# Optimization experiments

Hardware: AMD Instinct MI355X
Metric: run time of the kernel (lower is better)

The kernel has to match this reference:

```python
import jax, jax.numpy as jnp
import numpy as np
import math

V, D, H, NH, LE, LD = 32000, 256, 1024, 8, 2, 2
B, T = 4, 512


def qlinear(x, W, b):
    # x: [..., Din, 4]; W: [4, Dout, Din] (r,i,j,k); b: [Dout, 4] or None
    r, i, j, k = x[..., 0], x[..., 1], x[..., 2], x[..., 3]
    Wr, Wi, Wj, Wk = W[0], W[1], W[2], W[3]
    f = lambda a, M: jnp.einsum('...d,od->...o', a, M)
    ro = f(r, Wr) - f(i, Wi) - f(j, Wj) - f(k, Wk)
    io = f(r, Wi) + f(i, Wr) + f(j, Wk) - f(k, Wj)
    jo = f(r, Wj) - f(i, Wk) + f(j, Wr) + f(k, Wi)
    ko = f(r, Wk) + f(i, Wj) - f(j, Wi) + f(k, Wr)
    out = jnp.stack([ro, io, jo, ko], axis=-1)
    return out + b if b is not None else out


def modrelu(x, bias):
    # x: [..., F, 4]; bias: [F]
    norm = jnp.linalg.norm(x, axis=-1)
    scale = jax.nn.relu(norm + bias) / (norm + 1e-6)
    return x * scale[..., None]


def qnorm(x, g, beta):
    # normalize each quaternion (last dim of size 4) to unit norm
    n = jnp.sqrt(jnp.sum(x * x, axis=-1, keepdims=True) + 1e-6)
    return g * (x / n) + beta


def qattn(q, k, v, W, b, mask, nh):
    # W: [4(proj q,k,v,out), 4(comp), D, D]; b: [4, D, 4]
    def split(x):
        Bq, Tq, Dq, _ = x.shape
        return x.reshape(Bq, Tq, nh, Dq // nh, 4).transpose(0, 2, 1, 3, 4)
    qh = split(qlinear(q, W[0], b[0]))
    kh = split(qlinear(k, W[1], b[1]))
    vh = split(qlinear(v, W[2], b[2]))
    hd = qh.shape[3]
    s = jnp.einsum('bhqfd,bhkfd->bhqk', qh, kh) / math.sqrt(hd * 4)
    if mask is not None:
        s = jnp.where(mask[:, None] == 0, -jnp.inf, s)
    w = jax.nn.softmax(s, axis=-1)
    o = jnp.einsum('bhqk,bhkfd->bhqfd', w, vh)
    Bq, h, Tq, f, _ = o.shape
    o = o.transpose(0, 2, 1, 3, 4).reshape(Bq, Tq, h * f, 4)
    return qlinear(o, W[3], b[3])


def qff(x, W1, b1, mbias, W2, b2):
    return qlinear(modrelu(qlinear(x, W1, b1), mbias), W2, b2)


def qembed(ids, emb):
    d = emb.shape[-1]
    scale = 1.0 / 10000.0 ** (jnp.arange(d, dtype=jnp.float32) / d)
    r = emb[0][ids]
    i = emb[1][ids] * scale
    j = emb[2][ids] * scale
    k = emb[3][ids] * scale
    n = jnp.sqrt(r * r + i * i + j * j + k * k + 1e-6)
    return jnp.stack([r / n, i / n, j / n, k / n], axis=-1)


def rope(x):
    t, d = x.shape[1], x.shape[2]
    inv = 1.0 / 10000.0 ** (jnp.arange(0, d, 2, dtype=jnp.float32) / d)
    fr = jnp.arange(t, dtype=jnp.float32)[:, None] * inv[None, :]
    ang = jnp.concatenate([jnp.sin(fr), jnp.cos(fr)], axis=-1)  # [T, D]
    return x * ang[None, :, :, None]


def setup_inputs():
    key = jax.random.key(0)
    ks = jax.random.split(key, 12)
    n = lambda k, s: jax.random.normal(k, s, jnp.float32) * 0.02
    src = jax.random.randint(ks[0], (B, T), 0, V)
    tgt = jax.random.randint(ks[1], (B, T), 0, V)
    tgt_mask = jnp.broadcast_to(jnp.tril(jnp.ones((T, T), jnp.int32)), (B, T, T))
    return dict(
        src=src, tgt=tgt, tgt_mask=tgt_mask,
        emb=n(ks[2], (4, V, D)),
        enc_attn_W=n(ks[3], (LE, 4, 4, D, D)), enc_attn_b=jnp.zeros((LE, 4, D, 4)),
        enc_norm_g=jnp.ones((LE, 2, D, 4)), enc_norm_b=jnp.zeros((LE, 2, D, 4)),
        enc_ff_W1=n(ks[4], (LE, 4, H, D)), enc_ff_b1=jnp.zeros((LE, H, 4)),
        enc_ff_mod=jnp.zeros((LE, H)),
        enc_ff_W2=n(ks[5], (LE, 4, D, H)), enc_ff_b2=jnp.zeros((LE, D, 4)),
        dec_sa_W=n(ks[6], (LD, 4, 4, D, D)), dec_sa_b=jnp.zeros((LD, 4, D, 4)),
        dec_ca_W=n(ks[7], (LD, 4, 4, D, D)), dec_ca_b=jnp.zeros((LD, 4, D, 4)),
        dec_norm_g=jnp.ones((LD, 3, D, 4)), dec_norm_b=jnp.zeros((LD, 3, D, 4)),
        dec_ff_W1=n(ks[8], (LD, 4, H, D)), dec_ff_b1=jnp.zeros((LD, H, 4)),
        dec_ff_mod=jnp.zeros((LD, H)),
        dec_ff_W2=n(ks[9], (LD, 4, D, H)), dec_ff_b2=jnp.zeros((LD, D, 4)),
        fc_W=n(ks[10], (V, D)), fc_b=jnp.zeros((V,)),
    )


def reference(src, tgt, tgt_mask, emb,
              enc_attn_W, enc_attn_b, enc_norm_g, enc_norm_b,
              enc_ff_W1, enc_ff_b1, enc_ff_mod, enc_ff_W2, enc_ff_b2,
              dec_sa_W, dec_sa_b, dec_ca_W, dec_ca_b, dec_norm_g, dec_norm_b,
              dec_ff_W1, dec_ff_b1, dec_ff_mod, dec_ff_W2, dec_ff_b2,
              fc_W, fc_b):
    x_src = rope(qembed(src, emb))
    x_tgt = rope(qembed(tgt, emb))
    # encoder stack
    m = x_src
    for l in range(LE):
        m = qnorm(m + qattn(m, m, m, enc_attn_W[l], enc_attn_b[l], None, NH), enc_norm_g[l, 0], enc_norm_b[l, 0])
        m = qnorm(m + qff(m, enc_ff_W1[l], enc_ff_b1[l], enc_ff_mod[l], enc_ff_W2[l], enc_ff_b2[l]), enc_norm_g[l, 1], enc_norm_b[l, 1])
    # decoder stack
    x = x_tgt
    for l in range(LD):
        x = qnorm(x + qattn(x, x, x, dec_sa_W[l], dec_sa_b[l], tgt_mask, NH), dec_norm_g[l, 0], dec_norm_b[l, 0])
        x = qnorm(x + qattn(x, m, m, dec_ca_W[l], dec_ca_b[l], None, NH), dec_norm_g[l, 1], dec_norm_b[l, 1])
        x = qnorm(x + qff(x, dec_ff_W1[l], dec_ff_b1[l], dec_ff_mod[l], dec_ff_W2[l], dec_ff_b2[l]), dec_norm_g[l, 2], dec_norm_b[l, 2])
    real = jnp.linalg.norm(x, axis=-1)  # QuaternionToReal('norm') -> [B, T, D]
    logits = jnp.einsum('btd,vd->btv', real, fc_W) + fc_b
    return logits
```

## Files before the change

kernel.cpp:

```cpp
#include <hip/hip_runtime.h>
#include <math.h>

#define B 4
#define T 512
#define D 256
#define H 1024
#define NH 8
#define V 32000
#define BT (B*T)
#define LE 2
#define LD 2
#define DIM 1024

typedef __attribute__((ext_vector_type(8))) short s16x8;
typedef __attribute__((ext_vector_type(4))) float f32x4;
typedef __attribute__((address_space(3))) void lds_void;
typedef const __attribute__((address_space(1))) void g_void;

__device__ __forceinline__ ushort f2bf(float x) {
  uint u = __float_as_uint(x);
  return (ushort)((u + 0x7fffu + ((u >> 16) & 1u)) >> 16);
}
__device__ __forceinline__ float bf2f(ushort u) {
  return __uint_as_float(((uint)u) << 16);
}

#define QSCALE 0.08838834764831845f

#define A_CNT  1572864
#define F_CNT  2097152
#define FC_CNT 2048000
#define EMB_CNT (2 * BT * 256)
#define MEGA_TOT (A_CNT + F_CNT + FC_CNT + EMB_CNT)
#define WSTEP  1048576
#define FFW    4194304

__device__ __forceinline__ void qexpand_write(
    const float* __restrict__ src, ushort* __restrict__ dst,
    int o, int d, int Din, int P) {
  float w0 = src[(size_t)o * Din + d];
  float w1 = src[P + (size_t)o * Din + d];
  float w2 = src[2 * (size_t)P + (size_t)o * Din + d];
  float w3 = src[3 * (size_t)P + (size_t)o * Din + d];
  int K4 = Din * 4;
  size_t rbase = (size_t)(o * 4) * K4 + d * 4;
  *(ushort4*)(dst + rbase)          = make_ushort4(f2bf(w0), f2bf(-w1), f2bf(-w2), f2bf(-w3));
  *(ushort4*)(dst + rbase + K4)     = make_ushort4(f2bf(w1), f2bf(w0),  f2bf(w3),  f2bf(-w2));
  *(ushort4*)(dst + rbase + 2 * K4) = make_ushort4(f2bf(w2), f2bf(-w3), f2bf(w0),  f2bf(w1));
  *(ushort4*)(dst + rbase + 3 * K4) = make_ushort4(f2bf(w3), f2bf(w2),  f2bf(-w1), f2bf(w0));
}

__global__ __launch_bounds__(256) void mega_expand_kernel(
    const float* __restrict__ encA, const float* __restrict__ decSA,
    const float* __restrict__ decCA,
    const float* __restrict__ eW1, const float* __restrict__ eW2,
    const float* __restrict__ dW1, const float* __restrict__ dW2,
    const float* __restrict__ fcW,
    ushort* __restrict__ WA, ushort* __restrict__ WF, ushort* __restrict__ Wfc,
    const int* __restrict__ srcIds, const int* __restrict__ tgtIds,
    const float* __restrict__ emb,
    float* __restrict__ xsrc, ushort* __restrict__ xbfs,
    float* __restrict__ xtgt, ushort* __restrict__ xbft) {
  int gid = blockIdx.x * 256 + threadIdx.x;
  if (gid < A_CNT) {
    int u = gid >> 18;
    int p = (gid >> 16) & 3;
    int rem = gid & 65535;
    int o = rem >> 8, d = rem & 255;
    const float* base = (u < 2) ? encA + (size_t)u * 1048576
                      : (u < 4) ? decSA + (size_t)(u - 2) * 1048576
                                : decCA + (size_t)(u - 4) * 1048576;
    qexpand_write(base + (size_t)p * 262144,
                  WA + ((size_t)u * 4 + p) * WSTEP, o, d, 256, 65536);
  } else if (gid < A_CNT + F_CNT) {
    int idx = gid - A_CNT;
    int layer = idx >> 19;
    int w12 = (idx >> 18) & 1;
    int rem = idx & 262143;
    const float* w1b = (layer < 2) ? eW1 + (size_t)layer * 1048576
                                   : dW1 + (size_t)(layer - 2) * 1048576;
    const float* w2b = (layer < 2) ? eW2 + (size_t)layer * 1048576
                                   : dW2 + (size_t)(layer - 2) * 1048576;
    ushort* dst = WF + (size_t)layer * 2 * FFW + (size_t)w12 * FFW;
    if (w12 == 0) {
      int o = rem >> 8, d = rem & 255;
      qexpand_write(w1b, dst, o, d, 256, 262144);
    } else {
      int o = rem >> 10, d = rem & 1023;
      qexpand_write(w2b, dst, o, d, 1024, 262144);
    }
  } else if (gid < A_CNT + F_CNT + FC_CNT) {
    int idx = gid - A_CNT - F_CNT;
    float4 v = ((const float4*)fcW)[idx];
    ((ushort4*)Wfc)[idx] = make_ushort4(f2bf(v.x), f2bf(v.y), f2bf(v.z), f2bf(v.w));
  } else if (gid < MEGA_TOT) {
    int idx = gid - A_CNT - F_CNT - FC_CNT;
    int g = idx >> 8, d = idx & 255;
    int isTgt = g >= BT;
    int bt = isTgt ? g - BT : g;
    int id = isTgt ? tgtIds[bt] : srcIds[bt];
    float* out = isTgt ? xtgt : xsrc;
    ushort* outbf = isTgt ? xbft : xbfs;
    int t = bt % T;
    size_t VD = (size_t)V * D;
    float scale = powf(10000.f, -(float)d / (float)D);
    float r = emb[(size_t)id * D + d];
    float i = emb[VD + (size_t)id * D + d] * scale;
    float j = emb[2 * VD + (size_t)id * D + d] * scale;
    float k = emb[3 * VD + (size_t)id * D + d] * scale;
    float n = sqrtf(r * r + i * i + j * j + k * k + 1e-6f);
    float ang;
    if (d < D / 2) {
      float inv = powf(10000.f, -(float)(2 * d) / (float)D);
      ang = sinf((float)t * inv);
    } else {
      float inv = powf(10000.f, -(float)(2 * (d - D / 2)) / (float)D);
      ang = cosf((float)t * inv);
    }
    float s = ang / n;
    size_t base = (size_t)bt * DIM + d * 4;
    float4 q = make_float4(r * s, i * s, j * s, k * s);
    *(float4*)(out + base) = q;
    *(ushort4*)(outbf + base) = make_ushort4(f2bf(q.x), f2bf(q.y), f2bf(q.z), f2bf(q.w));
  }
}

struct GP {
  const ushort* A; const ushort* Aalt; int altStart;
  const ushort* Bt; const float* bias; void* Cv;
  ushort* qo; ushort* ko; ushort* vo;
  float* xres; ushort* xbf; const float* gg; const float* bb;
  const float* modb; ushort* realout;
};

template <int OMODE, int TM, int NBUF>
__global__ __launch_bounds__(256, 4) void gemm_bf16_kernel(
    GP u0, GP u1, int nunits, int nsplit, int N, int K) {
  __shared__ ushort As[NBUF][TM * 32];
  __shared__ ushort Bs[NBUF][128 * 32];
  const int tid = threadIdx.x;
  const int w = tid >> 6, l = tid & 63;
  const int nwg = gridDim.x;
  const int qq = nwg >> 3, rr = nwg & 7;
  const int xcd = blockIdx.x & 7, pos = blockIdx.x >> 3;
  const int wg = (xcd < rr ? xcd * (qq + 1) : rr * (qq + 1) + (xcd - rr) * qq) + pos;
  const int uwg = nwg / (nunits * nsplit);
  const int idx = wg / uwg;
  const int unit = idx / nsplit;
  const int split = idx % nsplit;
  const int wgl = wg % uwg;
  GP U = unit ? u1 : u0;
  const int Ksub = K / nsplit;
  const int kbase = split * Ksub;
  const int nbx = N >> 7;
  const int nby = uwg / nbx;
  const int m0 = (wgl % nby) * TM, n0 = (wgl / nby) * 128;
  const ushort* Ap = (U.altStart && n0 >= U.altStart) ? U.Aalt : U.A;
  const ushort* Btp = U.Bt;
  const int lr = l & 15, lg = l >> 4;
  constexpr int NR = (TM == 128) ? 4 : 2;
  const int wm = (TM == 128) ? (w >> 1) : 0;
  const int wn = (TM == 128) ? (w & 1) : w;
  const int wcol = wn * (NR * 16);
  f32x4 acc[4][NR] = {};
  const int NT = Ksub >> 5;

  auto stage = [&](int t, int buf) {
    int k0 = kbase + (t << 5);
#pragma unroll
    for (int s = 0; s < TM / 64; ++s) {
      int fb = (w * (TM / 64) + s) * 1024;
      int f = fb + l * 16;
      int row = f >> 6, cb = (f & 63) >> 1;
      __builtin_amdgcn_global_load_lds(
          (g_void*)(Ap + (size_t)(m0 + row) * K + k0 + cb),
          (lds_void*)((char*)&As[buf][0] + fb), 16, 0, 0);
    }
#pragma unroll
    for (int s = 0; s < 2; ++s) {
      int fb = (w * 2 + s) * 1024;
      int f = fb + l * 16;
      int row = f >> 6, cb = (f & 63) >> 1;
      __builtin_amdgcn_global_load_lds(
          (g_void*)(Btp + (size_t)(n0 + row) * K + k0 + cb),
          (lds_void*)((char*)&Bs[buf][0] + fb), 16, 0, 0);
    }
  };
  auto compute = [&](int buf) {
    s16x8 af[4], bfr[NR];
#pragma unroll
    for (int mi = 0; mi < 4; ++mi)
      af[mi] = *(const s16x8*)(&As[buf][0] + (wm * 64 + mi * 16 + lr) * 32 + lg * 8);
#pragma unroll
    for (int ni = 0; ni < NR; ++ni)
      bfr[ni] = *(const s16x8*)(&Bs[buf][0] + (wcol + ni * 16 + lr) * 32 + lg * 8);
    __builtin_amdgcn_s_setprio(1);
#pragma unroll
    for (int mi = 0; mi < 4; ++mi)
#pragma unroll
      for (int ni = 0; ni < NR; ++ni)
        acc[mi][ni] = __builtin_amdgcn_mfma_f32_16x16x32_bf16(af[mi], bfr[ni], acc[mi][ni], 0, 0, 0);
    __builtin_amdgcn_s_setprio(0);
  };

  if constexpr (NBUF == 4) {
    stage(0, 0);
    stage(1, 1);
    __syncthreads();
    for (int t = 0; t < NT; t += 2) {
      if (t + 2 < NT) {
        stage(t + 2, (t + 2) & 3);
        stage(t + 3, (t + 3) & 3);
      }
      compute(t & 3);
      compute((t + 1) & 3);
      __syncthreads();
    }
  } else {
    stage(0, 0);
    __syncthreads();
    int cur = 0;
    for (int t = 0; t < NT; ++t) {
      if (t + 1 < NT) stage(t + 1, cur ^ 1);
      compute(cur);
      __syncthreads();
      cur ^= 1;
    }
  }

#pragma unroll
  for (int mi = 0; mi < 4; ++mi) {
#pragma unroll
    for (int ni = 0; ni < NR; ++ni) {
      int row = m0 + wm * 64 + mi * 16 + lg * 4;
      int col = n0 + wcol + ni * 16 + lr;
      f32x4 v = acc[mi][ni];
      if constexpr (OMODE == 0) {
        float bv = U.bias ? U.bias[col] : 0.f;
        float* C = (float*)U.Cv;
#pragma unroll
        for (int r = 0; r < 4; ++r)
          C[(size_t)(row + r) * N + col] = v[r] + bv;
      } else if constexpr (OMODE == 3) {
        float bv = U.bias[col];
        if (col < 2048) {
          ushort* dst = (col < DIM) ? U.qo : U.ko;
          float sc = (col < DIM) ? QSCALE : 1.f;
          int c = col & (DIM - 1);
#pragma unroll
          for (int r = 0; r < 4; ++r)
            dst[(size_t)(row + r) * DIM + c] = f2bf((v[r] + bv) * sc);
        } else {
          int c = col - 2048;
          ushort4 o4 = make_ushort4(f2bf(v[0] + bv), f2bf(v[1] + bv),
                                    f2bf(v[2] + bv), f2bf(v[3] + bv));
          *(ushort4*)&U.vo[((size_t)((row >> 9) << 10) + c) * T + (row & 511)] = o4;
        }
      } else if constexpr (OMODE == 4) {
        float bv = U.bias[col];
        float gv = U.gg[col], bev = U.bb[col];
#pragma unroll
        for (int r = 0; r < 4; ++r) {
          float val = v[r] + bv + U.xres[(size_t)(row + r) * DIM + col];
          float sq = val * val;
          sq += __shfl_xor(sq, 1);
          sq += __shfl_xor(sq, 2);
          float invn = rsqrtf(sq + 1e-6f);
          float res = gv * (val * invn) + bev;
          U.xres[(size_t)(row + r) * DIM + col] = res;
          U.xbf[(size_t)(row + r) * DIM + col] = f2bf(res);
          if (U.realout) {
            float rsq = res * res;
            rsq += __shfl_xor(rsq, 1);
            rsq += __shfl_xor(rsq, 2);
            if ((col & 3) == 0)
              U.realout[(size_t)(row + r) * D + (col >> 2)] = f2bf(sqrtf(rsq));
          }
        }
      } else if constexpr (OMODE == 5) {
        float bv = U.bias[col];
        float mb = U.modb[col >> 2];
        ushort* C = (ushort*)U.Cv;
#pragma unroll
        for (int r = 0; r < 4; ++r) {
          float val = v[r] + bv;
          float sq = val * val;
          sq += __shfl_xor(sq, 1);
          sq += __shfl_xor(sq, 2);
          float norm = sqrtf(sq);
          float scale = fmaxf(norm + mb, 0.f) / (norm + 1e-6f);
          C[(size_t)(row + r) * N + col] = f2bf(val * scale);
        }
      } else {
        ushort* P = (ushort*)U.Cv + (size_t)split * BT * N;
#pragma unroll
        for (int r = 0; r < 4; ++r)
          P[(size_t)(row + r) * N + col] = f2bf(v[r]);
      }
    }
  }
}

__global__ __launch_bounds__(256) void ff2_merge_kernel(
    const ushort* __restrict__ P, const float* __restrict__ bias,
    float* __restrict__ xres, ushort* __restrict__ xbf,
    const float* __restrict__ gg, const float* __restrict__ bb,
    ushort* __restrict__ realo) {
  int idx = blockIdx.x * 256 + threadIdx.x;
  int row = idx >> 8;
  int c4 = (idx & 255) << 2;
  size_t base = (size_t)row * DIM + c4;
  float a0 = 0.f, a1 = 0.f, a2 = 0.f, a3 = 0.f;
#pragma unroll
  for (int sp = 0; sp < 4; ++sp) {
    ushort4 p = *(const ushort4*)(P + (size_t)sp * BT * DIM + base);
    a0 += bf2f(p.x); a1 += bf2f(p.y); a2 += bf2f(p.z); a3 += bf2f(p.w);
  }
  float4 xv = *(float4*)(xres + base);
  float v0 = a0 + bias[c4 + 0] + xv.x;
  float v1 = a1 + bias[c4 + 1] + xv.y;
  float v2 = a2 + bias[c4 + 2] + xv.z;
  float v3 = a3 + bias[c4 + 3] + xv.w;
  float invn = rsqrtf(v0 * v0 + v1 * v1 + v2 * v2 + v3 * v3 + 1e-6f);
  float r0 = gg[c4 + 0] * (v0 * invn) + bb[c4 + 0];
  float r1 = gg[c4 + 1] * (v1 * invn) + bb[c4 + 1];
  float r2 = gg[c4 + 2] * (v2 * invn) + bb[c4 + 2];
  float r3 = gg[c4 + 3] * (v3 * invn) + bb[c4 + 3];
  *(float4*)(xres + base) = make_float4(r0, r1, r2, r3);
  *(ushort4*)(xbf + base) = make_ushort4(f2bf(r0), f2bf(r1), f2bf(r2), f2bf(r3));
  if (realo)
    realo[(size_t)row * D + (c4 >> 2)] =
        f2bf(sqrtf(r0 * r0 + r1 * r1 + r2 * r2 + r3 * r3));
}

__global__ __launch_bounds__(256) void fused_attn_kernel(
    const ushort* __restrict__ qb, const ushort* __restrict__ kb,
    const ushort* __restrict__ vT, ushort* __restrict__ outA,
    int c0, int c1) {
  __shared__ ushort Ks[2][64 * 128];
  __shared__ ushort Vs[2][128 * 64];
  __shared__ ushort Pst[4][1024];
  const int tid = threadIdx.x;
  const int wq = tid >> 6, l = tid & 63;
  const int lr = l & 15, lg = l >> 4;
  const int h = blockIdx.y;
  const int u = blockIdx.z >> 2, b = blockIdx.z & 3;
  const size_t uoff = (size_t)u * ((size_t)BT * DIM);
  const int causal = u ? c1 : c0;
  const int q0 = blockIdx.x * 64 + wq * 16;
  const size_t bT = (size_t)b * T;
  const int hc = h * 128;
  const size_t vrow0 = (size_t)(b * NH + h) * 128;
  const ushort* qbu = qb + uoff;
  const ushort* kbu = kb + uoff;
  const ushort* vTu = vT + uoff;
  ushort* outu = outA + uoff;
  s16x8 qf[4];
#pragma unroll
  for (int ks = 0; ks < 4; ++ks)
    qf[ks] = *(const s16x8*)(qbu + (bT + q0 + lr) * DIM + hc + ks * 32 + lg * 8);
  f32x4 O[8] = {};
  float m[4] = {-3e38f, -3e38f, -3e38f, -3e38f};
  float lac[4] = {0.f, 0.f, 0.f, 0.f};
  const int kend = causal ? (blockIdx.x + 1) * 64 : T;
  const int ntile = kend >> 6;

  auto stageKV = [&](int tile, int buf) {
    int kv0 = tile << 6;
#pragma unroll
    for (int s = 0; s < 4; ++s) {
      int f = s * 4096 + tid * 16;
      int row = f >> 8, g = (f >> 4) & 15;
      int gs = g ^ (row & 7);
      __builtin_amdgcn_global_load_lds(
          (g_void*)(kbu + (bT + kv0 + row) * DIM + hc + gs * 8),
          (lds_void*)((char*)&Ks[buf][0] + f), 16, 0, 0);
    }
#pragma unroll
    for (int s = 0; s < 4; ++s) {
      int f = s * 4096 + tid * 16;
      int row = f >> 7, g = (f >> 4) & 7;
      int gs = g ^ (row & 7);
      __builtin_amdgcn_global_load_lds(
          (g_void*)(vTu + (vrow0 + row) * T + kv0 + gs * 8),
          (lds_void*)((char*)&Vs[buf][0] + f), 16, 0, 0);
    }
  };

  stageKV(0, 0);
  __syncthreads();
  int cur = 0;
  for (int tile = 0; tile < ntile; ++tile) {
    const int kv0 = tile << 6;
    if (tile + 1 < ntile) stageKV(tile + 1, cur ^ 1);
    f32x4 s[4] = {};
#pragma unroll
    for (int ks = 0; ks < 4; ++ks) {
      s16x8 kf[4];
#pragma unroll
      for (int ni = 0; ni < 4; ++ni) {
        int row = ni * 16 + lr;
        int g = (ks * 4 + lg) ^ (row & 7);
        kf[ni] = *(const s16x8*)(&Ks[cur][0] + row * 128 + g * 8);
      }
#pragma unroll
      for (int ni = 0; ni < 4; ++ni)
        s[ni] = __builtin_amdgcn_mfma_f32_16x16x32_bf16(qf[ks], kf[ni], s[ni], 0, 0, 0);
    }
    const bool domask = causal && (kv0 + 63 > q0);
#pragma unroll
    for (int r = 0; r < 4; ++r) {
      const int qrow = q0 + lg * 4 + r;
      float mx = -3e38f;
#pragma unroll
      for (int ni = 0; ni < 4; ++ni) {
        float v = s[ni][r];
        if (domask && (kv0 + ni * 16 + lr > qrow)) v = -3e38f;
        s[ni][r] = v;
        mx = fmaxf(mx, v);
      }
#pragma unroll
      for (int dd = 1; dd < 16; dd <<= 1) mx = fmaxf(mx, __shfl_xor(mx, dd));
      if (__ballot(mx > m[r] + 8.f)) {
        float mn = fmaxf(m[r], mx);
        float alpha = __expf(m[r] - mn);
        m[r] = mn;
        lac[r] *= alpha;
#pragma unroll
        for (int dni = 0; dni < 8; ++dni) O[dni][r] *= alpha;
      }
      float ps = 0.f;
#pragma unroll
      for (int ni = 0; ni < 4; ++ni) {
        float p = __expf(s[ni][r] - m[r]);
        s[ni][r] = p;
        ps += p;
      }
#pragma unroll
      for (int dd = 1; dd < 16; dd <<= 1) ps += __shfl_xor(ps, dd);
      lac[r] += ps;
      const int qloc = lg * 4 + r;
      const int sw = (qloc & 7) << 3;
#pragma unroll
      for (int ni = 0; ni < 4; ++ni)
        Pst[wq][qloc * 64 + ((ni * 16 + lr) ^ sw)] = f2bf(s[ni][r]);
    }
    asm volatile("s_waitcnt lgkmcnt(0)" ::: "memory");
    __builtin_amdgcn_sched_barrier(0);
#pragma unroll
    for (int ks2 = 0; ks2 < 2; ++ks2) {
      s16x8 pa = *(const s16x8*)&Pst[wq][lr * 64 + ((ks2 * 32 + lg * 8) ^ ((lr & 7) << 3))];
#pragma unroll
      for (int dni = 0; dni < 8; ++dni) {
        int row = dni * 16 + lr;
        int g = (ks2 * 4 + lg) ^ (row & 7);
        s16x8 vf = *(const s16x8*)(&Vs[cur][0] + row * 64 + g * 8);
        O[dni] = __builtin_amdgcn_mfma_f32_16x16x32_bf16(pa, vf, O[dni], 0, 0, 0);
      }
    }
    __syncthreads();
    cur ^= 1;
  }
#pragma unroll
  for (int r = 0; r < 4; ++r) {
    float inv = 1.f / lac[r];
    const size_t row = bT + q0 + lg * 4 + r;
#pragma unroll
    for (int dni = 0; dni < 8; ++dni)
      outu[row * DIM + hc + dni * 16 + lr] = f2bf(O[dni][r] * inv);
  }
}

extern "C" void kernel_launch(void* const* d_in, const int* in_sizes, int n_in,
                              void* d_out, int out_size, void* d_ws, size_t ws_size,
                              hipStream_t stream) {
  const int*   src        = (const int*)d_in[0];
  const int*   tgt        = (const int*)d_in[1];
  const float* emb        = (const float*)d_in[3];
  const float* enc_attn_W = (const float*)d_in[4];
  const float* enc_attn_b = (const float*)d_in[5];
  const float* enc_norm_g = (const float*)d_in[6];
  const float* enc_norm_b = (const float*)d_in[7];
  const float* enc_ff_W1  = (const float*)d_in[8];
  const float* enc_ff_b1  = (const float*)d_in[9];
  const float* enc_ff_mod = (const float*)d_in[10];
  const float* enc_ff_W2  = (const float*)d_in[11];
  const float* enc_ff_b2  = (const float*)d_in[12];
  const float* dec_sa_W   = (const float*)d_in[13];
  const float* dec_sa_b   = (const float*)d_in[14];
  const float* dec_ca_W   = (const float*)d_in[15];
  const float* dec_ca_b   = (const float*)d_in[16];
  const float* dec_norm_g = (const float*)d_in[17];
  const float* dec_norm_b = (const float*)d_in[18];
  const float* dec_ff_W1  = (const float*)d_in[19];
  const float* dec_ff_b1  = (const float*)d_in[20];
  const float* dec_ff_mod = (const float*)d_in[21];
  const float* dec_ff_W2  = (const float*)d_in[22];
  const float* dec_ff_b2  = (const float*)d_in[23];
  const float* fc_W       = (const float*)d_in[24];
  const float* fc_b       = (const float*)d_in[25];
  float* out = (float*)d_out;

  const size_t USZ = (size_t)BT * DIM;
  float* ws    = (float*)d_ws;
  float* xsrc  = ws;
  float* xtgt  = xsrc + USZ;
  ushort* xbf_src = (ushort*)(xtgt + USZ);
  ushort* xbf_tgt = xbf_src + USZ;
  ushort* aobf    = xbf_tgt + USZ;
  ushort* qb      = aobf + 2 * USZ;
  ushort* kb      = qb + 2 * USZ;
  ushort* vTb     = kb + 2 * USZ;
  ushort* hbf     = vTb + 2 * USZ;
  ushort* realbf  = hbf + (size_t)BT * H * 4;
  ushort* WA      = realbf + (size_t)BT * D;
  ushort* WF      = WA + (size_t)6 * 4 * WSTEP;
  ushort* Wfc     = WF + (size_t)4 * 2 * FFW;
  ushort* Pff     = Wfc + (size_t)V * D;

  mega_expand_kernel<<<(MEGA_TOT + 255) / 256, 256, 0, stream>>>(
      enc_attn_W, dec_sa_W, dec_ca_W,
      enc_ff_W1, enc_ff_W2, dec_ff_W1, dec_ff_W2, fc_W, WA, WF, Wfc,
      src, tgt, emb, xsrc, xbf_src, xtgt, xbf_tgt);

  GP Z{};

  auto mkQKV = [&](const ushort* Abf, const ushort* Wu, const float* bb, int u) {
    GP g = Z;
    g.A = Abf; g.Bt = Wu; g.bias = bb;
    g.qo = qb + u * USZ; g.ko = kb + u * USZ; g.vo = vTb + u * USZ;
    return g;
  };
  auto mkOP = [&](int u, const ushort* Wu3, const float* bb, float* xres,
                  ushort* xbf, const float* gg, const float* nb, ushort* realo) {
    GP g = Z;
    g.A = aobf + u * USZ; g.Bt = Wu3; g.bias = bb;
    g.xres = xres; g.xbf = xbf; g.gg = gg; g.bb = nb; g.realout = realo;
    return g;
  };

  auto qkv1 = [&](GP g) {
    gemm_bf16_kernel<3, 128, 2><<<384, 256, 0, stream>>>(g, g, 1, 1, 3 * DIM, DIM);
  };
  auto qkv2 = [&](GP g0, GP g1) {
    gemm_bf16_kernel<3, 128, 2><<<768, 256, 0, stream>>>(g0, g1, 2, 1, 3 * DIM, DIM);
  };
  auto op1 = [&](GP g) {
    gemm_bf16_kernel<4, 64, 4><<<256, 256, 0, stream>>>(g, g, 1, 1, DIM, DIM);
  };
  auto op2 = [&](GP g0, GP g1) {
    gemm_bf16_kernel<4, 64, 4><<<512, 256, 0, stream>>>(g0, g1, 2, 1, DIM, DIM);
  };
  auto attn1 = [&](int causal) {
    fused_attn_kernel<<<dim3(T / 64, NH, B), 256, 0, stream>>>(
        qb, kb, vTb, aobf, causal, causal);
  };
  auto ffpair = [&](const ushort* xbf, int layer, const float* b1,
                    const float* mod, const float* b2, float* xres,
                    ushort* xbfo, const float* gg, const float* nb,
                    ushort* realo) {
    const ushort* Wf = WF + (size_t)layer * 2 * FFW;
    GP g1 = Z;
    g1.A = xbf; g1.Bt = Wf; g1.bias = b1; g1.Cv = hbf; g1.modb = mod;
    gemm_bf16_kernel<5, 128, 2><<<512, 256, 0, stream>>>(g1, g1, 1, 1, 4 * H, DIM);
    GP g2 = Z;
    g2.A = hbf; g2.Bt = Wf + FFW; g2.Cv = Pff;
    gemm_bf16_kernel<6, 64, 2><<<1024, 256, 0, stream>>>(g2, g2, 1, 4, DIM, 4 * H);
    ff2_merge_kernel<<<BT, 256, 0, stream>>>(Pff, b2, xres, xbfo, gg, nb, realo);
  };

  {
    GP e = mkQKV(xbf_src, WA + (size_t)(0 * 4) * WSTEP, enc_attn_b, 0);
    GP d = mkQKV(xbf_tgt, WA + (size_t)(2 * 4) * WSTEP, dec_sa_b, 1);
    qkv2(e, d);
    fused_attn_kernel<<<dim3(T / 64, NH, 2 * B), 256, 0, stream>>>(
        qb, kb, vTb, aobf, 0, 1);
    GP eo = mkOP(0, WA + (size_t)(0 * 4 + 3) * WSTEP, enc_attn_b + 3 * DIM,
                 xsrc, xbf_src, enc_norm_g, enc_norm_b, nullptr);
    GP dd = mkOP(1, WA + (size_t)(2 * 4 + 3) * WSTEP, dec_sa_b + 3 * DIM,
                 xtgt, xbf_tgt, dec_norm_g, dec_norm_b, nullptr);
    op2(eo, dd);
  }
  ffpair(xbf_src, 0, enc_ff_b1, enc_ff_mod, enc_ff_b2, xsrc, xbf_src,
         enc_norm_g + 1 * DIM, enc_norm_b + 1 * DIM, nullptr);
  {
    GP e = mkQKV(xbf_src, WA + (size_t)(1 * 4) * WSTEP,
                 enc_attn_b + (size_t)1 * 4 * DIM, 0);
    qkv1(e);
    attn1(0);
    GP eo = mkOP(0, WA + (size_t)(1 * 4 + 3) * WSTEP,
                 enc_attn_b + (size_t)1 * 4 * DIM + 3 * DIM,
                 xsrc, xbf_src, enc_norm_g + 2 * DIM, enc_norm_b + 2 * DIM, nullptr);
    op1(eo);
  }
  ffpair(xbf_src, 1, enc_ff_b1 + (size_t)1 * H * 4, enc_ff_mod + H,
         enc_ff_b2 + DIM, xsrc, xbf_src,
         enc_norm_g + 3 * DIM, enc_norm_b + 3 * DIM, nullptr);

  for (int l = 0; l < LD; ++l) {
    if (l > 0) {
      GP d = mkQKV(xbf_tgt, WA + (size_t)((2 + l) * 4) * WSTEP,
                   dec_sa_b + (size_t)l * 4 * DIM, 0);
      qkv1(d);
      attn1(1);
      GP od = mkOP(0, WA + (size_t)((2 + l) * 4 + 3) * WSTEP,
                   dec_sa_b + (size_t)l * 4 * DIM + 3 * DIM,
                   xtgt, xbf_tgt, dec_norm_g + (size_t)(l * 3) * DIM,
                   dec_norm_b + (size_t)(l * 3) * DIM, nullptr);
      op1(od);
    }
    {
      GP g = mkQKV(xbf_tgt, WA + (size_t)((4 + l) * 4) * WSTEP,
                   dec_ca_b + (size_t)l * 4 * DIM, 0);
      g.Aalt = xbf_src; g.altStart = DIM;
      qkv1(g);
      attn1(0);
      GP og = mkOP(0, WA + (size_t)((4 + l) * 4 + 3) * WSTEP,
                   dec_ca_b + (size_t)l * 4 * DIM + 3 * DIM,
                   xtgt, xbf_tgt, dec_norm_g + (size_t)(l * 3 + 1) * DIM,
                   dec_norm_b + (size_t)(l * 3 + 1) * DIM, nullptr);
      op1(og);
    }
    ffpair(xbf_tgt, 2 + l, dec_ff_b1 + (size_t)l * H * 4,
           dec_ff_mod + (size_t)l * H, dec_ff_b2 + (size_t)l * DIM,
           xtgt, xbf_tgt, dec_norm_g + (size_t)(l * 3 + 2) * DIM,
           dec_norm_b + (size_t)(l * 3 + 2) * DIM,
           (l == LD - 1) ? realbf : nullptr);
  }

  {
    GP g = Z;
    g.A = realbf; g.Bt = Wfc; g.bias = fc_b; g.Cv = out;
    gemm_bf16_kernel<0, 128, 2><<<(V / 128) * (BT / 128), 256, 0, stream>>>(
        g, g, 1, 1, V, 256);
  }
}
```

Measured before the change: 961.7 us.

## Split-K the attention output projection and move residual qnorm into a merge kernel

The attention output-projection GEMM no longer fuses bias, residual and quaternion norm into its epilogue. It now runs as a 4-way split-K GEMM that writes bf16 partial sums, followed by a merge kernel that sums the partials and applies the residual qnorm. That merge kernel can also handle two units in one launch. The aim is more workgroups and better occupancy for the K=1024 projection, and the separate 4-buffer pipeline variant of the GEMM is dropped. The cost is extra global traffic for the partials, an extra launch per projection, bf16 rounding of the partials, and the dual-unit path needs the partial buffer to hold 8 slices.

```diff
diff --git a/kernel.cpp b/kernel.cpp
--- a/kernel.cpp
+++ b/kernel.cpp
@@ -129,15 +129,14 @@
   const ushort* A; const ushort* Aalt; int altStart;
   const ushort* Bt; const float* bias; void* Cv;
   ushort* qo; ushort* ko; ushort* vo;
-  float* xres; ushort* xbf; const float* gg; const float* bb;
-  const float* modb; ushort* realout;
+  const float* modb;
 };
 
-template <int OMODE, int TM, int NBUF>
+template <int OMODE, int TM>
 __global__ __launch_bounds__(256, 4) void gemm_bf16_kernel(
     GP u0, GP u1, int nunits, int nsplit, int N, int K) {
-  __shared__ ushort As[NBUF][TM * 32];
-  __shared__ ushort Bs[NBUF][128 * 32];
+  __shared__ ushort As[2][TM * 32];
+  __shared__ ushort Bs[2][128 * 32];
   const int tid = threadIdx.x;
   const int w = tid >> 6, l = tid & 63;
   const int nwg = gridDim.x;
@@ -203,29 +202,14 @@
     __builtin_amdgcn_s_setprio(0);
   };
 
-  if constexpr (NBUF == 4) {
-    stage(0, 0);
-    stage(1, 1);
+  stage(0, 0);
+  __syncthreads();
+  int cur = 0;
+  for (int t = 0; t < NT; ++t) {
+    if (t + 1 < NT) stage(t + 1, cur ^ 1);
+    compute(cur);
     __syncthreads();
-    for (int t = 0; t < NT; t += 2) {
-      if (t + 2 < NT) {
-        stage(t + 2, (t + 2) & 3);
-        stage(t + 3, (t + 3) & 3);
-      }
-      compute(t & 3);
-      compute((t + 1) & 3);
-      __syncthreads();
-    }
-  } else {
-    stage(0, 0);
-    __syncthreads();
-    int cur = 0;
-    for (int t = 0; t < NT; ++t) {
-      if (t + 1 < NT) stage(t + 1, cur ^ 1);
-      compute(cur);
-      __syncthreads();
-      cur ^= 1;
-    }
+    cur ^= 1;
   }
 
 #pragma unroll
@@ -255,27 +239,6 @@
           ushort4 o4 = make_ushort4(f2bf(v[0] + bv), f2bf(v[1] + bv),
                                     f2bf(v[2] + bv), f2bf(v[3] + bv));
           *(ushort4*)&U.vo[((size_t)((row >> 9) << 10) + c) * T + (row & 511)] = o4;
-        }
-      } else if constexpr (OMODE == 4) {
-        float bv = U.bias[col];
-        float gv = U.gg[col], bev = U.bb[col];
-#pragma unroll
-        for (int r = 0; r < 4; ++r) {
-          float val = v[r] + bv + U.xres[(size_t)(row + r) * DIM + col];
-          float sq = val * val;
-          sq += __shfl_xor(sq, 1);
-          sq += __shfl_xor(sq, 2);
-          float invn = rsqrtf(sq + 1e-6f);
-          float res = gv * (val * invn) + bev;
-          U.xres[(size_t)(row + r) * DIM + col] = res;
-          U.xbf[(size_t)(row + r) * DIM + col] = f2bf(res);
-          if (U.realout) {
-            float rsq = res * res;
-            rsq += __shfl_xor(rsq, 1);
-            rsq += __shfl_xor(rsq, 2);
-            if ((col & 3) == 0)
-              U.realout[(size_t)(row + r) * D + (col >> 2)] = f2bf(sqrtf(rsq));
-          }
         }
       } else if constexpr (OMODE == 5) {
         float bv = U.bias[col];
@@ -301,35 +264,38 @@
   }
 }
 
-__global__ __launch_bounds__(256) void ff2_merge_kernel(
-    const ushort* __restrict__ P, const float* __restrict__ bias,
-    float* __restrict__ xres, ushort* __restrict__ xbf,
-    const float* __restrict__ gg, const float* __restrict__ bb,
-    ushort* __restrict__ realo) {
-  int idx = blockIdx.x * 256 + threadIdx.x;
-  int row = idx >> 8;
-  int c4 = (idx & 255) << 2;
+struct MP {
+  const ushort* P; const float* bias;
+  float* xres; ushort* xbf;
+  const float* gg; const float* bb; ushort* realo;
+};
+
+__global__ __launch_bounds__(256) void merge_qnorm_kernel(MP m0, MP m1) {
+  int blk = blockIdx.x;
+  MP M = (blk >= BT) ? m1 : m0;
+  int row = (blk >= BT) ? blk - BT : blk;
+  int c4 = threadIdx.x << 2;
   size_t base = (size_t)row * DIM + c4;
   float a0 = 0.f, a1 = 0.f, a2 = 0.f, a3 = 0.f;
 #pragma unroll
   for (int sp = 0; sp < 4; ++sp) {
-    ushort4 p = *(const ushort4*)(P + (size_t)sp * BT * DIM + base);
+    ushort4 p = *(const ushort4*)(M.P + (size_t)sp * BT * DIM + base);
     a0 += bf2f(p.x); a1 += bf2f(p.y); a2 += bf2f(p.z); a3 += bf2f(p.w);
   }
-  float4 xv = *(float4*)(xres + base);
-  float v0 = a0 + bias[c4 + 0] + xv.x;
-  float v1 = a1 + bias[c4 + 1] + xv.y;
-  float v2 = a2 + bias[c4 + 2] + xv.z;
-  float v3 = a3 + bias[c4 + 3] + xv.w;
+  float4 xv = *(float4*)(M.xres + base);
+  float v0 = a0 + M.bias[c4 + 0] + xv.x;
+  float v1 = a1 + M.bias[c4 + 1] + xv.y;
+  float v2 = a2 + M.bias[c4 + 2] + xv.z;
+  float v3 = a3 + M.bias[c4 + 3] + xv.w;
   float invn = rsqrtf(v0 * v0 + v1 * v1 + v2 * v2 + v3 * v3 + 1e-6f);
-  float r0 = gg[c4 + 0] * (v0 * invn) + bb[c4 + 0];
-  float r1 = gg[c4 + 1] * (v1 * invn) + bb[c4 + 1];
-  float r2 = gg[c4 + 2] * (v2 * invn) + bb[c4 + 2];
-  float r3 = gg[c4 + 3] * (v3 * invn) + bb[c4 + 3];
-  *(float4*)(xres + base) = make_float4(r0, r1, r2, r3);
-  *(ushort4*)(xbf + base) = make_ushort4(f2bf(r0), f2bf(r1), f2bf(r2), f2bf(r3));
-  if (realo)
-    realo[(size_t)row * D + (c4 >> 2)] =
+  float r0 = M.gg[c4 + 0] * (v0 * invn) + M.bb[c4 + 0];
+  float r1 = M.gg[c4 + 1] * (v1 * invn) + M.bb[c4 + 1];
+  float r2 = M.gg[c4 + 2] * (v2 * invn) + M.bb[c4 + 2];
+  float r3 = M.gg[c4 + 3] * (v3 * invn) + M.bb[c4 + 3];
+  *(float4*)(M.xres + base) = make_float4(r0, r1, r2, r3);
+  *(ushort4*)(M.xbf + base) = make_ushort4(f2bf(r0), f2bf(r1), f2bf(r2), f2bf(r3));
+  if (M.realo)
+    M.realo[(size_t)row * D + (c4 >> 2)] =
         f2bf(sqrtf(r0 * r0 + r1 * r1 + r2 * r2 + r3 * r3));
 }
 
@@ -524,6 +490,7 @@
       src, tgt, emb, xsrc, xbf_src, xtgt, xbf_tgt);
 
   GP Z{};
+  MP MZ{};
 
   auto mkQKV = [&](const ushort* Abf, const ushort* Wu, const float* bb, int u) {
     GP g = Z;
@@ -531,25 +498,32 @@
     g.qo = qb + u * USZ; g.ko = kb + u * USZ; g.vo = vTb + u * USZ;
     return g;
   };
-  auto mkOP = [&](int u, const ushort* Wu3, const float* bb, float* xres,
-                  ushort* xbf, const float* gg, const float* nb, ushort* realo) {
+  auto mkMP = [&](const ushort* P, const float* bb, float* xres, ushort* xbf,
+                  const float* gg, const float* nb, ushort* realo) {
+    MP m = MZ;
+    m.P = P; m.bias = bb; m.xres = xres; m.xbf = xbf;
+    m.gg = gg; m.bb = nb; m.realo = realo;
+    return m;
+  };
+
+  auto qkv1 = [&](GP g) {
+    gemm_bf16_kernel<3, 128><<<384, 256, 0, stream>>>(g, g, 1, 1, 3 * DIM, DIM);
+  };
+  auto qkv2 = [&](GP g0, GP g1) {
+    gemm_bf16_kernel<3, 128><<<768, 256, 0, stream>>>(g0, g1, 2, 1, 3 * DIM, DIM);
+  };
+  auto op1 = [&](int u, const ushort* Wu3, MP m) {
     GP g = Z;
-    g.A = aobf + u * USZ; g.Bt = Wu3; g.bias = bb;
-    g.xres = xres; g.xbf = xbf; g.gg = gg; g.bb = nb; g.realout = realo;
-    return g;
-  };
-
-  auto qkv1 = [&](GP g) {
-    gemm_bf16_kernel<3, 128, 2><<<384, 256, 0, stream>>>(g, g, 1, 1, 3 * DIM, DIM);
-  };
-  auto qkv2 = [&](GP g0, GP g1) {
-    gemm_bf16_kernel<3, 128, 2><<<768, 256, 0, stream>>>(g0, g1, 2, 1, 3 * DIM, DIM);
-  };
-  auto op1 = [&](GP g) {
-    gemm_bf16_kernel<4, 64, 4><<<256, 256, 0, stream>>>(g, g, 1, 1, DIM, DIM);
-  };
-  auto op2 = [&](GP g0, GP g1) {
-    gemm_bf16_kernel<4, 64, 4><<<512, 256, 0, stream>>>(g0, g1, 2, 1, DIM, DIM);
+    g.A = aobf + u * USZ; g.Bt = Wu3; g.Cv = Pff;
+    gemm_bf16_kernel<6, 64><<<1024, 256, 0, stream>>>(g, g, 1, 4, DIM, DIM);
+    merge_qnorm_kernel<<<BT, 256, 0, stream>>>(m, m);
+  };
+  auto op2 = [&](const ushort* We3, const ushort* Wd3, MP me, MP md) {
+    GP g0 = Z, g1 = Z;
+    g0.A = aobf; g0.Bt = We3; g0.Cv = Pff;
+    g1.A = aobf + USZ; g1.Bt = Wd3; g1.Cv = Pff + 4 * USZ;
+    gemm_bf16_kernel<6, 64><<<2048, 256, 0, stream>>>(g0, g1, 2, 4, DIM, DIM);
+    merge_qnorm_kernel<<<2 * BT, 256, 0, stream>>>(me, md);
   };
   auto attn1 = [&](int causal) {
     fused_attn_kernel<<<dim3(T / 64, NH, B), 256, 0, stream>>>(
@@ -562,11 +536,12 @@
     const ushort* Wf = WF + (size_t)layer * 2 * FFW;
     GP g1 = Z;
     g1.A = xbf; g1.Bt = Wf; g1.bias = b1; g1.Cv = hbf; g1.modb = mod;
-    gemm_bf16_kernel<5, 128, 2><<<512, 256, 0, stream>>>(g1, g1, 1, 1, 4 * H, DIM);
+    gemm_bf16_kernel<5, 128><<<512, 256, 0, stream>>>(g1, g1, 1, 1, 4 * H, DIM);
     GP g2 = Z;
     g2.A = hbf; g2.Bt = Wf + FFW; g2.Cv = Pff;
-    gemm_bf16_kernel<6, 64, 2><<<1024, 256, 0, stream>>>(g2, g2, 1, 4, DIM, 4 * H);
-    ff2_merge_kernel<<<BT, 256, 0, stream>>>(Pff, b2, xres, xbfo, gg, nb, realo);
+    gemm_bf16_kernel<6, 64><<<1024, 256, 0, stream>>>(g2, g2, 1, 4, DIM, 4 * H);
+    MP m = mkMP(Pff, b2, xres, xbfo, gg, nb, realo);
+    merge_qnorm_kernel<<<BT, 256, 0, stream>>>(m, m);
   };
 
   {
@@ -575,11 +550,11 @@
     qkv2(e, d);
     fused_attn_kernel<<<dim3(T / 64, NH, 2 * B), 256, 0, stream>>>(
         qb, kb, vTb, aobf, 0, 1);
-    GP eo = mkOP(0, WA + (size_t)(0 * 4 + 3) * WSTEP, enc_attn_b + 3 * DIM,
-                 xsrc, xbf_src, enc_norm_g, enc_norm_b, nullptr);
-    GP dd = mkOP(1, WA + (size_t)(2 * 4 + 3) * WSTEP, dec_sa_b + 3 * DIM,
-                 xtgt, xbf_tgt, dec_norm_g, dec_norm_b, nullptr);
-    op2(eo, dd);
+    MP me = mkMP(Pff, enc_attn_b + 3 * DIM, xsrc, xbf_src,
+                 enc_norm_g, enc_norm_b, nullptr);
+    MP md = mkMP(Pff + 4 * USZ, dec_sa_b + 3 * DIM, xtgt, xbf_tgt,
+                 dec_norm_g, dec_norm_b, nullptr);
+    op2(WA + (size_t)(0 * 4 + 3) * WSTEP, WA + (size_t)(2 * 4 + 3) * WSTEP, me, md);
   }
   ffpair(xbf_src, 0, enc_ff_b1, enc_ff_mod, enc_ff_b2, xsrc, xbf_src,
          enc_norm_g + 1 * DIM, enc_norm_b + 1 * DIM, nullptr);
@@ -588,10 +563,9 @@
                  enc_attn_b + (size_t)1 * 4 * DIM, 0);
     qkv1(e);
     attn1(0);
-    GP eo = mkOP(0, WA + (size_t)(1 * 4 + 3) * WSTEP,
-                 enc_attn_b + (size_t)1 * 4 * DIM + 3 * DIM,
-                 xsrc, xbf_src, enc_norm_g + 2 * DIM, enc_norm_b + 2 * DIM, nullptr);
-    op1(eo);
+    MP me = mkMP(Pff, enc_attn_b + (size_t)1 * 4 * DIM + 3 * DIM, xsrc, xbf_src,
+                 enc_norm_g + 2 * DIM, enc_norm_b + 2 * DIM, nullptr);
+    op1(0, WA + (size_t)(1 * 4 + 3) * WSTEP, me);
   }
   ffpair(xbf_src, 1, enc_ff_b1 + (size_t)1 * H * 4, enc_ff_mod + H,
          enc_ff_b2 + DIM, xsrc, xbf_src,
@@ -603,11 +577,10 @@
                    dec_sa_b + (size_t)l * 4 * DIM, 0);
       qkv1(d);
       attn1(1);
-      GP od = mkOP(0, WA + (size_t)((2 + l) * 4 + 3) * WSTEP,
-                   dec_sa_b + (size_t)l * 4 * DIM + 3 * DIM,
-                   xtgt, xbf_tgt, dec_norm_g + (size_t)(l * 3) * DIM,
+      MP md = mkMP(Pff, dec_sa_b + (size_t)l * 4 * DIM + 3 * DIM, xtgt, xbf_tgt,
+                   dec_norm_g + (size_t)(l * 3) * DIM,
                    dec_norm_b + (size_t)(l * 3) * DIM, nullptr);
-      op1(od);
+      op1(0, WA + (size_t)((2 + l) * 4 + 3) * WSTEP, md);
     }
     {
       GP g = mkQKV(xbf_tgt, WA + (size_t)((4 + l) * 4) * WSTEP,
@@ -615,11 +588,10 @@
       g.Aalt = xbf_src; g.altStart = DIM;
       qkv1(g);
       attn1(0);
-      GP og = mkOP(0, WA + (size_t)((4 + l) * 4 + 3) * WSTEP,
-                   dec_ca_b + (size_t)l * 4 * DIM + 3 * DIM,
-                   xtgt, xbf_tgt, dec_norm_g + (size_t)(l * 3 + 1) * DIM,
+      MP mg = mkMP(Pff, dec_ca_b + (size_t)l * 4 * DIM + 3 * DIM, xtgt, xbf_tgt,
+                   dec_norm_g + (size_t)(l * 3 + 1) * DIM,
                    dec_norm_b + (size_t)(l * 3 + 1) * DIM, nullptr);
-      op1(og);
+      op1(0, WA + (size_t)((4 + l) * 4 + 3) * WSTEP, mg);
     }
     ffpair(xbf_tgt, 2 + l, dec_ff_b1 + (size_t)l * H * 4,
            dec_ff_mod + (size_t)l * H, dec_ff_b2 + (size_t)l * DIM,
@@ -631,7 +603,7 @@
   {
     GP g = Z;
     g.A = realbf; g.Bt = Wfc; g.bias = fc_b; g.Cv = out;
-    gemm_bf16_kernel<0, 128, 2><<<(V / 128) * (BT / 128), 256, 0, stream>>>(
+    gemm_bf16_kernel<0, 128><<<(V / 128) * (BT / 128), 256, 0, stream>>>(
         g, g, 1, 1, V, 256);
   }
 }
```

Result: faster. 930.3 us (median of 2 runs) (-3.3%).
